# Optimization experiments

Measured on AMD Instinct MI355X. Metric: run time of the kernel, lower is better.

Reference implementation:

```python
import jax, jax.numpy as jnp
import numpy as np

CUTOFF = 5.0
N = 8192
BOX = 55.0


def setup_inputs() -> dict:
    key = jax.random.key(0)
    xyz = jax.random.uniform(key, (N, 3), dtype=jnp.float32) * BOX
    cell = jnp.diag(jnp.full((3,), BOX, dtype=jnp.float32))  # [3,3] box vectors (rows)
    ii, jj = np.triu_indices(N, k=1)  # all i<j candidate pairs, P = N*(N-1)/2
    return {
        "xyz": xyz,
        "cell": cell,
        "idx_i": jnp.asarray(ii, dtype=jnp.int32),
        "idx_j": jnp.asarray(jj, dtype=jnp.int32),
    }


def _min_image_deltas(xyz, cell, idx_i, idx_j):
    # [P,3] raw displacement for every candidate pair
    delta = xyz[idx_i] - xyz[idx_j]
    # triclinic minimum-image reduction, z -> y -> x order (NNPOps convention)
    delta = delta - jnp.round(delta[:, 2:3] / cell[2, 2]) * cell[2]
    delta = delta - jnp.round(delta[:, 1:2] / cell[1, 1]) * cell[1]
    delta = delta - jnp.round(delta[:, 0:1] / cell[0, 0]) * cell[0]
    dist = jnp.sqrt(jnp.sum(delta * delta, axis=1))  # [P]
    return delta, dist


def reference(xyz, cell, idx_i, idx_j):
    delta, dist = _min_image_deltas(xyz, cell, idx_i, idx_j)
    mask = dist < CUTOFF  # [P] bool
    # neighbors: -1 marks pairs beyond cutoff (fixed-shape output, jit-safe)
    pair_i = jnp.where(mask, idx_i, jnp.int32(-1))
    pair_j = jnp.where(mask, idx_j, jnp.int32(-1))
    pair_diff = jnp.where(mask[:, None], delta, jnp.float32(0.0))  # [P,3]
    pair_dist = jnp.where(mask, dist, jnp.float32(0.0))  # [P]
    return pair_i, pair_j, pair_diff, pair_dist
```

## Files before the change

kernel.cpp:

```cpp
#include <hip/hip_runtime.h>
#include <math.h>


#define NL_CUTOFF 5.0f

__device__ __forceinline__ void solve_ij(long long p, int N, int& io, int& jo) {
    const double A = (double)(2 * N - 1);
    double disc = A * A - 8.0 * (double)p;
    long long ii = (long long)((A - sqrt(disc)) * 0.5);
    if (ii < 0) ii = 0;
    if (ii > N - 2) ii = N - 2;
    while (ii > 0 && (ii * (2LL * N - 1 - ii)) >> 1 > p) --ii;
    while (((ii + 1) * (2LL * N - 1 - (ii + 1))) >> 1 <= p) ++ii;
    const long long off = (ii * (2LL * N - 1 - ii)) >> 1;
    io = (int)ii;
    jo = (int)(p - off + ii + 1);
}

struct CellC {
    float r0x, r0y, r0z, rc0;
    float r1x, r1y, r1z, rc1;
    float r2x, r2y, r2z, rc2;
};

__device__ __forceinline__ void pair_compute(
    const float* __restrict__ xyz, const CellC& c,
    int ii, int jj,
    float& oi, float& oj, float& odx, float& ody, float& odz, float& orr)
{
    float dx = __fsub_rn(xyz[3 * ii + 0], xyz[3 * jj + 0]);
    float dy = __fsub_rn(xyz[3 * ii + 1], xyz[3 * jj + 1]);
    float dz = __fsub_rn(xyz[3 * ii + 2], xyz[3 * jj + 2]);

    float s = rintf(__fmul_rn(dz, c.rc2));
    dx = __fsub_rn(dx, __fmul_rn(s, c.r2x));
    dy = __fsub_rn(dy, __fmul_rn(s, c.r2y));
    dz = __fsub_rn(dz, __fmul_rn(s, c.r2z));

    s = rintf(__fmul_rn(dy, c.rc1));
    dx = __fsub_rn(dx, __fmul_rn(s, c.r1x));
    dy = __fsub_rn(dy, __fmul_rn(s, c.r1y));
    dz = __fsub_rn(dz, __fmul_rn(s, c.r1z));

    s = rintf(__fmul_rn(dx, c.rc0));
    dx = __fsub_rn(dx, __fmul_rn(s, c.r0x));
    dy = __fsub_rn(dy, __fmul_rn(s, c.r0y));
    dz = __fsub_rn(dz, __fmul_rn(s, c.r0z));

    float ss = __fadd_rn(__fadd_rn(__fmul_rn(dx, dx), __fmul_rn(dy, dy)),
                         __fmul_rn(dz, dz));
    float r = __fsqrt_rn(ss);
    bool m = (r < NL_CUTOFF);

    oi  = m ? (float)ii : -1.0f;
    oj  = m ? (float)jj : -1.0f;
    odx = m ? dx : 0.0f;
    ody = m ? dy : 0.0f;
    odz = m ? dz : 0.0f;
    orr = m ? r  : 0.0f;
}

__global__ __launch_bounds__(256) void nl_kernel(
    const float* __restrict__ xyz,
    const float* __restrict__ cell,
    float* __restrict__ out,
    long long P, int N)
{
    CellC c;
    c.r0x = cell[0]; c.r0y = cell[1]; c.r0z = cell[2];
    c.r1x = cell[3]; c.r1y = cell[4]; c.r1z = cell[5];
    c.r2x = cell[6]; c.r2y = cell[7]; c.r2z = cell[8];
    c.rc0 = __fdiv_rn(1.0f, c.r0x);
    c.rc1 = __fdiv_rn(1.0f, c.r1y);
    c.rc2 = __fdiv_rn(1.0f, c.r2z);

    float* __restrict__ out_i = out;
    float* __restrict__ out_j = out + P;
    float* __restrict__ out_d = out + 2 * P;
    float* __restrict__ out_r = out + 5 * P;

    const long long nquad  = P >> 2;
    const long long stride = (long long)gridDim.x * blockDim.x;
    const long long tid0   = (long long)blockIdx.x * blockDim.x + threadIdx.x;

    for (long long q = tid0; q < nquad; q += stride) {
        int i, j;
        solve_ij(q << 2, N, i, j);

        float oia[4], oja[4], ora[4], od[12];
#pragma unroll
        for (int k = 0; k < 4; ++k) {
            pair_compute(xyz, c, i, j,
                         oia[k], oja[k], od[3 * k + 0], od[3 * k + 1],
                         od[3 * k + 2], ora[k]);
            if (++j >= N) { ++i; j = i + 1; }
        }

        ((float4*)out_i)[q] = make_float4(oia[0], oia[1], oia[2], oia[3]);
        ((float4*)out_j)[q] = make_float4(oja[0], oja[1], oja[2], oja[3]);
        ((float4*)out_r)[q] = make_float4(ora[0], ora[1], ora[2], ora[3]);
        float4* dd = (float4*)(out_d + 12 * q);
        dd[0] = make_float4(od[0], od[1],  od[2],  od[3]);
        dd[1] = make_float4(od[4], od[5],  od[6],  od[7]);
        dd[2] = make_float4(od[8], od[9],  od[10], od[11]);
    }

    for (long long p = (nquad << 2) + tid0; p < P; p += stride) {
        int i, j;
        solve_ij(p, N, i, j);
        float oi, oj, dx, dy, dz, rr;
        pair_compute(xyz, c, i, j, oi, oj, dx, dy, dz, rr);
        out_i[p] = oi;
        out_j[p] = oj;
        out_d[3 * p + 0] = dx;
        out_d[3 * p + 1] = dy;
        out_d[3 * p + 2] = dz;
        out_r[p] = rr;
    }
}

extern "C" void kernel_launch(void* const* d_in, const int* in_sizes, int n_in,
                              void* d_out, int out_size, void* d_ws, size_t ws_size,
                              hipStream_t stream) {
    const float* xyz  = (const float*)d_in[0];
    const float* cell = (const float*)d_in[1];
    float* out = (float*)d_out;

    const int       N = in_sizes[0] / 3;
    const long long P = (long long)in_sizes[2];

    const int block = 256;
    long long nquad = P >> 2;
    long long blocks_needed = (nquad + block - 1) / block;
    int grid = (int)(blocks_needed < 2048 ? (blocks_needed > 0 ? blocks_needed : 1)
                                          : 2048);

    nl_kernel<<<grid, block, 0, stream>>>(xyz, cell, out, P, N);
}
```

Baseline: 161.8 us.

## Assign one block per row i and pad coordinates to float4

Drops the per-quad double-precision sqrt inversion of pair index to (i,j). Each block now handles a single row i of the upper-triangle pair list, loading xi once and reading j coordinates from a float4-padded copy built by a small prepass kernel in the workspace. Row edges that are not quad-aligned are handled by per-thread scalar tails. The cost is an extra kernel launch plus N-1 blocks of very uneven size, with short rows leaving most threads idle.

```diff
diff --git a/kernel.cpp b/kernel.cpp
--- a/kernel.cpp
+++ b/kernel.cpp
@@ -4,17 +4,16 @@
 
 #define NL_CUTOFF 5.0f
 
-__device__ __forceinline__ void solve_ij(long long p, int N, int& io, int& jo) {
-    const double A = (double)(2 * N - 1);
-    double disc = A * A - 8.0 * (double)p;
-    long long ii = (long long)((A - sqrt(disc)) * 0.5);
-    if (ii < 0) ii = 0;
-    if (ii > N - 2) ii = N - 2;
-    while (ii > 0 && (ii * (2LL * N - 1 - ii)) >> 1 > p) --ii;
-    while (((ii + 1) * (2LL * N - 1 - (ii + 1))) >> 1 <= p) ++ii;
-    const long long off = (ii * (2LL * N - 1 - ii)) >> 1;
-    io = (int)ii;
-    jo = (int)(p - off + ii + 1);
+typedef float f32x4 __attribute__((ext_vector_type(4)));
+
+__global__ __launch_bounds__(256) void pad_xyz_kernel(
+    const float* __restrict__ xyz, float* __restrict__ xyz4, int N)
+{
+    int a = blockIdx.x * blockDim.x + threadIdx.x;
+    if (a < N) {
+        f32x4 v = { xyz[3 * a + 0], xyz[3 * a + 1], xyz[3 * a + 2], 0.0f };
+        ((f32x4*)xyz4)[a] = v;
+    }
 }
 
 struct CellC {
@@ -24,13 +23,13 @@
 };
 
 __device__ __forceinline__ void pair_compute(
-    const float* __restrict__ xyz, const CellC& c,
-    int ii, int jj,
+    float xi, float yi, float zi, float xj, float yj, float zj,
+    const CellC& c, int ii, int jj,
     float& oi, float& oj, float& odx, float& ody, float& odz, float& orr)
 {
-    float dx = __fsub_rn(xyz[3 * ii + 0], xyz[3 * jj + 0]);
-    float dy = __fsub_rn(xyz[3 * ii + 1], xyz[3 * jj + 1]);
-    float dz = __fsub_rn(xyz[3 * ii + 2], xyz[3 * jj + 2]);
+    float dx = __fsub_rn(xi, xj);
+    float dy = __fsub_rn(yi, yj);
+    float dz = __fsub_rn(zi, zj);
 
     float s = rintf(__fmul_rn(dz, c.rc2));
     dx = __fsub_rn(dx, __fmul_rn(s, c.r2x));
@@ -60,8 +59,8 @@
     orr = m ? r  : 0.0f;
 }
 
-__global__ __launch_bounds__(256) void nl_kernel(
-    const float* __restrict__ xyz,
+__global__ __launch_bounds__(256) void nl_row_kernel(
+    const float* __restrict__ xyz4,
     const float* __restrict__ cell,
     float* __restrict__ out,
     long long P, int N)
@@ -74,27 +73,42 @@
     c.rc1 = __fdiv_rn(1.0f, c.r1y);
     c.rc2 = __fdiv_rn(1.0f, c.r2z);
 
+    const int       i   = blockIdx.x;
+    const long long L   = (long long)(N - 1 - i);
+    const long long off = ((long long)i * (2LL * N - 1 - i)) >> 1;
+
+    const f32x4 pi = ((const f32x4*)xyz4)[i];
+    const float xi = pi.x, yi = pi.y, zi = pi.z;
+
     float* __restrict__ out_i = out;
     float* __restrict__ out_j = out + P;
     float* __restrict__ out_d = out + 2 * P;
     float* __restrict__ out_r = out + 5 * P;
 
-    const long long nquad  = P >> 2;
-    const long long stride = (long long)gridDim.x * blockDim.x;
-    const long long tid0   = (long long)blockIdx.x * blockDim.x + threadIdx.x;
+    long long qstart = (off + 3) >> 2;
+    long long qend   = (off + L) >> 2;
+    long long fq_lo, fq_hi;
+    if (qend > qstart) { fq_lo = qstart << 2; fq_hi = qend << 2; }
+    else { fq_lo = off; fq_hi = off; qstart = 0; qend = 0; }
 
-    for (long long q = tid0; q < nquad; q += stride) {
-        int i, j;
-        solve_ij(q << 2, N, i, j);
+    for (long long q = qstart + threadIdx.x; q < qend; q += blockDim.x) {
+        const long long p  = q << 2;
+        const int       j0 = i + 1 + (int)(p - off);
+
+        const f32x4 pj0 = ((const f32x4*)xyz4)[j0 + 0];
+        const f32x4 pj1 = ((const f32x4*)xyz4)[j0 + 1];
+        const f32x4 pj2 = ((const f32x4*)xyz4)[j0 + 2];
+        const f32x4 pj3 = ((const f32x4*)xyz4)[j0 + 3];
 
         float oia[4], oja[4], ora[4], od[12];
-#pragma unroll
-        for (int k = 0; k < 4; ++k) {
-            pair_compute(xyz, c, i, j,
-                         oia[k], oja[k], od[3 * k + 0], od[3 * k + 1],
-                         od[3 * k + 2], ora[k]);
-            if (++j >= N) { ++i; j = i + 1; }
-        }
+        pair_compute(xi, yi, zi, pj0.x, pj0.y, pj0.z, c, i, j0 + 0,
+                     oia[0], oja[0], od[0], od[1], od[2], ora[0]);
+        pair_compute(xi, yi, zi, pj1.x, pj1.y, pj1.z, c, i, j0 + 1,
+                     oia[1], oja[1], od[3], od[4], od[5], ora[1]);
+        pair_compute(xi, yi, zi, pj2.x, pj2.y, pj2.z, c, i, j0 + 2,
+                     oia[2], oja[2], od[6], od[7], od[8], ora[2]);
+        pair_compute(xi, yi, zi, pj3.x, pj3.y, pj3.z, c, i, j0 + 3,
+                     oia[3], oja[3], od[9], od[10], od[11], ora[3]);
 
         ((float4*)out_i)[q] = make_float4(oia[0], oia[1], oia[2], oia[3]);
         ((float4*)out_j)[q] = make_float4(oja[0], oja[1], oja[2], oja[3]);
@@ -105,11 +119,18 @@
         dd[2] = make_float4(od[8], od[9],  od[10], od[11]);
     }
 
-    for (long long p = (nquad << 2) + tid0; p < P; p += stride) {
-        int i, j;
-        solve_ij(p, N, i, j);
+    const long long ne1 = fq_lo - off;
+    const long long ne2 = (off + L) - fq_hi;
+    const long long t   = threadIdx.x;
+    long long p = -1;
+    if (t < ne1)            p = off + t;
+    else if (t < ne1 + ne2) p = fq_hi + (t - ne1);
+    if (p >= 0) {
+        const int j = i + 1 + (int)(p - off);
+        const f32x4 pj = ((const f32x4*)xyz4)[j];
         float oi, oj, dx, dy, dz, rr;
-        pair_compute(xyz, c, i, j, oi, oj, dx, dy, dz, rr);
+        pair_compute(xi, yi, zi, pj.x, pj.y, pj.z, c, i, j,
+                     oi, oj, dx, dy, dz, rr);
         out_i[p] = oi;
         out_j[p] = oj;
         out_d[3 * p + 0] = dx;
@@ -124,16 +145,12 @@
                               hipStream_t stream) {
     const float* xyz  = (const float*)d_in[0];
     const float* cell = (const float*)d_in[1];
-    float* out = (float*)d_out;
+    float* out  = (float*)d_out;
+    float* xyz4 = (float*)d_ws;
 
     const int       N = in_sizes[0] / 3;
     const long long P = (long long)in_sizes[2];
 
-    const int block = 256;
-    long long nquad = P >> 2;
-    long long blocks_needed = (nquad + block - 1) / block;
-    int grid = (int)(blocks_needed < 2048 ? (blocks_needed > 0 ? blocks_needed : 1)
-                                          : 2048);
-
-    nl_kernel<<<grid, block, 0, stream>>>(xyz, cell, out, P, N);
+    pad_xyz_kernel<<<(N + 255) / 256, 256, 0, stream>>>(xyz, xyz4, N);
+    nl_row_kernel<<<N - 1, 256, 0, stream>>>(xyz4, cell, out, P, N);
 }
```

New measurement: 214.6 us. +32.6%, slower.

## Use int/float pair index solve, diagonal-cell fast path, hoist i-atom loads

Applied to the files above, without the earlier changes.

Replaces the double-precision sqrt and 64-bit integer index recovery with 32-bit integer and float arithmetic. Adds a runtime check for a diagonal cell that selects a templated path skipping the off-diagonal minimum-image terms. In the common case where all four pairs share row i, atom i is loaded once and the j atoms are read consecutively. Float sqrt near large discriminants relies on the correction loops for exactness, and int products could overflow for larger N.

```diff
diff --git a/kernel.cpp b/kernel.cpp
--- a/kernel.cpp
+++ b/kernel.cpp
@@ -4,17 +4,17 @@
 
 #define NL_CUTOFF 5.0f
 
-__device__ __forceinline__ void solve_ij(long long p, int N, int& io, int& jo) {
-    const double A = (double)(2 * N - 1);
-    double disc = A * A - 8.0 * (double)p;
-    long long ii = (long long)((A - sqrt(disc)) * 0.5);
+__device__ __forceinline__ void solve_ij(int p, int N, int& io, int& jo) {
+    const int A = 2 * N - 1;
+    const int disc = A * A - 8 * p;
+    const float sd = __fsqrt_rn((float)disc);
+    int ii = (int)(__fmul_rn(__fsub_rn((float)A, sd), 0.5f));
     if (ii < 0) ii = 0;
     if (ii > N - 2) ii = N - 2;
-    while (ii > 0 && (ii * (2LL * N - 1 - ii)) >> 1 > p) --ii;
-    while (((ii + 1) * (2LL * N - 1 - (ii + 1))) >> 1 <= p) ++ii;
-    const long long off = (ii * (2LL * N - 1 - ii)) >> 1;
-    io = (int)ii;
-    jo = (int)(p - off + ii + 1);
+    while (ii > 0 && ((ii * (A - ii)) >> 1) > p) --ii;
+    while ((((ii + 1) * (A - ii - 1)) >> 1) <= p) ++ii;
+    io = ii;
+    jo = p - ((ii * (A - ii)) >> 1) + ii + 1;
 }
 
 struct CellC {
@@ -23,41 +23,120 @@
     float r2x, r2y, r2z, rc2;
 };
 
+template <bool DIAG>
 __device__ __forceinline__ void pair_compute(
-    const float* __restrict__ xyz, const CellC& c,
-    int ii, int jj,
+    float xi, float yi, float zi, float xj, float yj, float zj,
+    const CellC& c, float fi, float fj,
     float& oi, float& oj, float& odx, float& ody, float& odz, float& orr)
 {
-    float dx = __fsub_rn(xyz[3 * ii + 0], xyz[3 * jj + 0]);
-    float dy = __fsub_rn(xyz[3 * ii + 1], xyz[3 * jj + 1]);
-    float dz = __fsub_rn(xyz[3 * ii + 2], xyz[3 * jj + 2]);
+    float dx = __fsub_rn(xi, xj);
+    float dy = __fsub_rn(yi, yj);
+    float dz = __fsub_rn(zi, zj);
 
-    float s = rintf(__fmul_rn(dz, c.rc2));
-    dx = __fsub_rn(dx, __fmul_rn(s, c.r2x));
-    dy = __fsub_rn(dy, __fmul_rn(s, c.r2y));
-    dz = __fsub_rn(dz, __fmul_rn(s, c.r2z));
+    if (DIAG) {
+        float s = rintf(__fmul_rn(dz, c.rc2));
+        dz = __fsub_rn(dz, __fmul_rn(s, c.r2z));
+        s = rintf(__fmul_rn(dy, c.rc1));
+        dy = __fsub_rn(dy, __fmul_rn(s, c.r1y));
+        s = rintf(__fmul_rn(dx, c.rc0));
+        dx = __fsub_rn(dx, __fmul_rn(s, c.r0x));
+    } else {
+        float s = rintf(__fmul_rn(dz, c.rc2));
+        dx = __fsub_rn(dx, __fmul_rn(s, c.r2x));
+        dy = __fsub_rn(dy, __fmul_rn(s, c.r2y));
+        dz = __fsub_rn(dz, __fmul_rn(s, c.r2z));
 
-    s = rintf(__fmul_rn(dy, c.rc1));
-    dx = __fsub_rn(dx, __fmul_rn(s, c.r1x));
-    dy = __fsub_rn(dy, __fmul_rn(s, c.r1y));
-    dz = __fsub_rn(dz, __fmul_rn(s, c.r1z));
+        s = rintf(__fmul_rn(dy, c.rc1));
+        dx = __fsub_rn(dx, __fmul_rn(s, c.r1x));
+        dy = __fsub_rn(dy, __fmul_rn(s, c.r1y));
+        dz = __fsub_rn(dz, __fmul_rn(s, c.r1z));
 
-    s = rintf(__fmul_rn(dx, c.rc0));
-    dx = __fsub_rn(dx, __fmul_rn(s, c.r0x));
-    dy = __fsub_rn(dy, __fmul_rn(s, c.r0y));
-    dz = __fsub_rn(dz, __fmul_rn(s, c.r0z));
+        s = rintf(__fmul_rn(dx, c.rc0));
+        dx = __fsub_rn(dx, __fmul_rn(s, c.r0x));
+        dy = __fsub_rn(dy, __fmul_rn(s, c.r0y));
+        dz = __fsub_rn(dz, __fmul_rn(s, c.r0z));
+    }
 
     float ss = __fadd_rn(__fadd_rn(__fmul_rn(dx, dx), __fmul_rn(dy, dy)),
                          __fmul_rn(dz, dz));
     float r = __fsqrt_rn(ss);
     bool m = (r < NL_CUTOFF);
 
-    oi  = m ? (float)ii : -1.0f;
-    oj  = m ? (float)jj : -1.0f;
+    oi  = m ? fi : -1.0f;
+    oj  = m ? fj : -1.0f;
     odx = m ? dx : 0.0f;
     ody = m ? dy : 0.0f;
     odz = m ? dz : 0.0f;
     orr = m ? r  : 0.0f;
+}
+
+template <bool DIAG>
+__device__ __forceinline__ void nl_body(
+    const float* __restrict__ xyz, const CellC& c,
+    float* __restrict__ out, long long P, int N)
+{
+    float* __restrict__ out_i = out;
+    float* __restrict__ out_j = out + P;
+    float* __restrict__ out_d = out + 2 * P;
+    float* __restrict__ out_r = out + 5 * P;
+
+    const long long nquad  = P >> 2;
+    const long long stride = (long long)gridDim.x * blockDim.x;
+    const long long tid0   = (long long)blockIdx.x * blockDim.x + threadIdx.x;
+
+    for (long long q = tid0; q < nquad; q += stride) {
+        int i, j;
+        solve_ij((int)(q << 2), N, i, j);
+
+        float oia[4], oja[4], ora[4], od[12];
+        if (j + 3 <= N - 1) {
+            const float xi = xyz[3 * i + 0], yi = xyz[3 * i + 1], zi = xyz[3 * i + 2];
+            const float fi = (float)i, fj = (float)j;
+#pragma unroll
+            for (int k = 0; k < 4; ++k) {
+                pair_compute<DIAG>(xi, yi, zi,
+                                   xyz[3 * (j + k) + 0], xyz[3 * (j + k) + 1],
+                                   xyz[3 * (j + k) + 2],
+                                   c, fi, fj + (float)k,
+                                   oia[k], oja[k], od[3 * k + 0], od[3 * k + 1],
+                                   od[3 * k + 2], ora[k]);
+            }
+        } else {
+            int ii = i, jj = j;
+#pragma unroll
+            for (int k = 0; k < 4; ++k) {
+                pair_compute<DIAG>(xyz[3 * ii + 0], xyz[3 * ii + 1], xyz[3 * ii + 2],
+                                   xyz[3 * jj + 0], xyz[3 * jj + 1], xyz[3 * jj + 2],
+                                   c, (float)ii, (float)jj,
+                                   oia[k], oja[k], od[3 * k + 0], od[3 * k + 1],
+                                   od[3 * k + 2], ora[k]);
+                if (++jj >= N) { ++ii; jj = ii + 1; }
+            }
+        }
+
+        ((float4*)out_i)[q] = make_float4(oia[0], oia[1], oia[2], oia[3]);
+        ((float4*)out_j)[q] = make_float4(oja[0], oja[1], oja[2], oja[3]);
+        ((float4*)out_r)[q] = make_float4(ora[0], ora[1], ora[2], ora[3]);
+        float4* dd = (float4*)(out_d + 12 * q);
+        dd[0] = make_float4(od[0], od[1],  od[2],  od[3]);
+        dd[1] = make_float4(od[4], od[5],  od[6],  od[7]);
+        dd[2] = make_float4(od[8], od[9],  od[10], od[11]);
+    }
+
+    for (long long p = (nquad << 2) + tid0; p < P; p += stride) {
+        int i, j;
+        solve_ij((int)p, N, i, j);
+        float oi, oj, dx, dy, dz, rr;
+        pair_compute<DIAG>(xyz[3 * i + 0], xyz[3 * i + 1], xyz[3 * i + 2],
+                           xyz[3 * j + 0], xyz[3 * j + 1], xyz[3 * j + 2],
+                           c, (float)i, (float)j, oi, oj, dx, dy, dz, rr);
+        out_i[p] = oi;
+        out_j[p] = oj;
+        out_d[3 * p + 0] = dx;
+        out_d[3 * p + 1] = dy;
+        out_d[3 * p + 2] = dz;
+        out_r[p] = rr;
+    }
 }
 
 __global__ __launch_bounds__(256) void nl_kernel(
@@ -74,49 +153,12 @@
     c.rc1 = __fdiv_rn(1.0f, c.r1y);
     c.rc2 = __fdiv_rn(1.0f, c.r2z);
 
-    float* __restrict__ out_i = out;
-    float* __restrict__ out_j = out + P;
-    float* __restrict__ out_d = out + 2 * P;
-    float* __restrict__ out_r = out + 5 * P;
+    const bool diag = (c.r0y == 0.0f) && (c.r0z == 0.0f) &&
+                      (c.r1x == 0.0f) && (c.r1z == 0.0f) &&
+                      (c.r2x == 0.0f) && (c.r2y == 0.0f);
 
-    const long long nquad  = P >> 2;
-    const long long stride = (long long)gridDim.x * blockDim.x;
-    const long long tid0   = (long long)blockIdx.x * blockDim.x + threadIdx.x;
-
-    for (long long q = tid0; q < nquad; q += stride) {
-        int i, j;
-        solve_ij(q << 2, N, i, j);
-
-        float oia[4], oja[4], ora[4], od[12];
-#pragma unroll
-        for (int k = 0; k < 4; ++k) {
-            pair_compute(xyz, c, i, j,
-                         oia[k], oja[k], od[3 * k + 0], od[3 * k + 1],
-                         od[3 * k + 2], ora[k]);
-            if (++j >= N) { ++i; j = i + 1; }
-        }
-
-        ((float4*)out_i)[q] = make_float4(oia[0], oia[1], oia[2], oia[3]);
-        ((float4*)out_j)[q] = make_float4(oja[0], oja[1], oja[2], oja[3]);
-        ((float4*)out_r)[q] = make_float4(ora[0], ora[1], ora[2], ora[3]);
-        float4* dd = (float4*)(out_d + 12 * q);
-        dd[0] = make_float4(od[0], od[1],  od[2],  od[3]);
-        dd[1] = make_float4(od[4], od[5],  od[6],  od[7]);
-        dd[2] = make_float4(od[8], od[9],  od[10], od[11]);
-    }
-
-    for (long long p = (nquad << 2) + tid0; p < P; p += stride) {
-        int i, j;
-        solve_ij(p, N, i, j);
-        float oi, oj, dx, dy, dz, rr;
-        pair_compute(xyz, c, i, j, oi, oj, dx, dy, dz, rr);
-        out_i[p] = oi;
-        out_j[p] = oj;
-        out_d[3 * p + 0] = dx;
-        out_d[3 * p + 1] = dy;
-        out_d[3 * p + 2] = dz;
-        out_r[p] = rr;
-    }
+    if (diag) nl_body<true>(xyz, c, out, P, N);
+    else      nl_body<false>(xyz, c, out, P, N);
 }
 
 extern "C" void kernel_launch(void* const* d_in, const int* in_sizes, int n_in,
```

Result: slower. 165.7 us (+2.4%).
